# Kernel optimization log

Measured on AMD Instinct MI355X. Metric: run time of the kernel, lower is better.

The kernel has to match this reference:

```python
import jax, jax.numpy as jnp
import numpy as np

T, B, E, H = 2048, 2, 2048, 16
HD = E // H
SCALE = HD ** -0.5
NEG = -1e9  # large-negative additive mask (finite, safe in fp32/bf16)


def setup_inputs() -> dict:
    key = jax.random.key(0)
    ks = jax.random.split(key, 6)
    query = jax.random.normal(ks[0], (T, B, E), dtype=jnp.float32)
    # causal additive mask, as metaseq builds for decoder self-attention
    attn_mask = jnp.where(jnp.tril(jnp.ones((T, T), dtype=bool)), 0.0, NEG).astype(jnp.float32)
    # combined qkv projection: rows ordered [K | V | Q] per split_tensor_along_last_dim
    qkv_w = jax.random.normal(ks[1], (3 * E, E), dtype=jnp.float32) * (1.0 / np.sqrt(2 * E))
    qkv_b = jax.random.uniform(ks[2], (3 * E,), dtype=jnp.float32, minval=-1, maxval=1) / np.sqrt(E)
    out_w = jax.random.normal(ks[3], (E, E), dtype=jnp.float32) * (1.0 / np.sqrt(2 * E))
    out_b = jax.random.uniform(ks[4], (E,), dtype=jnp.float32, minval=-1, maxval=1) / np.sqrt(E)
    return {"query": query, "attn_mask": attn_mask, "qkv_w": qkv_w,
            "qkv_b": qkv_b, "out_w": out_w, "out_b": out_b}


def reference(query, attn_mask, qkv_w, qkv_b, out_w, out_b):
    t, b, e = query.shape
    # fused QKV projection (ColumnParallelLinear, world_size=1)
    kvq = jnp.einsum('tbe,fe->tbf', query, qkv_w) + qkv_b  # [T,B,3E]
    k, v, q = kvq[..., :e], kvq[..., e:2 * e], kvq[..., 2 * e:]
    q = q * SCALE
    q = q.reshape(t, b, H, HD)
    k = k.reshape(t, b, H, HD)
    v = v.reshape(t, b, H, HD)
    # explicit QK^T bmm -> [B,H,T,S]
    scores = jnp.einsum('tbhd,sbhd->bhts', q, k) + attn_mask[None, None]
    probs = jax.nn.softmax(scores, axis=-1)  # dropout p=0 -> identity
    ctx = jnp.einsum('bhts,sbhd->tbhd', probs, v).reshape(t, b, e)
    # RowParallelLinear out_proj (skip_bias_add in the original; bias added here)
    out = jnp.einsum('tbe,fe->tbf', ctx, out_w) + out_b
    return out
```

## Files before the change

### kernel.cpp

```cpp
#include <hip/hip_runtime.h>
#include <hip/hip_bf16.h>
#include <stdint.h>

#define T_DIM 2048
#define B_DIM 2
#define E_DIM 2048
#define H_DIM 16
#define HD_DIM 128
#define F_DIM 6144
#define F2   4096
#define ROWS 4096
#define KVB 64

#define QK_SCALE 0.08838834764831845f
#define LOG2E    1.4426950408889634f
#define RESCALE_THR 8.0f

typedef __bf16 bf16_t;
typedef __bf16 bf16x8 __attribute__((ext_vector_type(8)));
typedef __bf16 bf16x4 __attribute__((ext_vector_type(4)));
typedef float  f32x4  __attribute__((ext_vector_type(4)));

__device__ __forceinline__ void gll16(const void* g, void* l) {
  __builtin_amdgcn_global_load_lds((const __attribute__((address_space(1))) void*)g,
                                   (__attribute__((address_space(3))) void*)l, 16, 0, 0);
}

__global__ void cvt3(const float* __restrict__ s0, bf16_t* __restrict__ d0, int n0,
                     const float* __restrict__ s1, bf16_t* __restrict__ d1, int n1,
                     const float* __restrict__ s2, bf16_t* __restrict__ d2, int n2) {
  int total = n0 + n1 + n2;
  int i = blockIdx.x * blockDim.x + threadIdx.x;
  int stride = gridDim.x * blockDim.x;
  for (; i < total; i += stride) {
    const float* s; bf16_t* d; int j;
    if (i < n0)            { s = s0; d = d0; j = i; }
    else if (i < n0 + n1)  { s = s1; d = d1; j = i - n0; }
    else                   { s = s2; d = d2; j = i - n0 - n1; }
    float4 v = ((const float4*)s)[j];
    bf16x4 o;
    o[0] = (bf16_t)v.x; o[1] = (bf16_t)v.y; o[2] = (bf16_t)v.z; o[3] = (bf16_t)v.w;
    ((bf16x4*)d)[j] = o;
  }
}

__launch_bounds__(256, 2)
__global__ void gemm_qkv(const bf16_t* __restrict__ A, const bf16_t* __restrict__ Bm,
                         const float* __restrict__ bias, bf16_t* __restrict__ KVQ2,
                         bf16_t* __restrict__ VTg)
{
  __shared__ __align__(16) bf16_t Sm[2][128][64];
  bf16_t* Tp = &Sm[0][0][0];
  const int K = E_DIM, nbn = 48;

  int bid = blockIdx.x;
  int cpx = gridDim.x >> 3;
  int swz = (bid & 7) * cpx + (bid >> 3);
  int bm = swz / nbn, bn = swz % nbn;

  int tid = threadIdx.x;
  int lane = tid & 63, wid = tid >> 6;
  int lr = lane & 15, lg = lane >> 4;
  int wm = wid >> 1, wn = wid & 1;

  f32x4 acc[4][4] = {};

  int srow8 = tid >> 3;
  int schunk = tid & 7;

  const bf16_t* gA = A + (size_t)(bm * 128) * K;
  const bf16_t* gB = Bm + (size_t)(bn * 128) * K;

  for (int k0 = 0; k0 < K; k0 += 64) {
    #pragma unroll
    for (int i = 0; i < 4; ++i) {
      int row = i * 32 + srow8;
      int sc = schunk ^ (row & 7);
      gll16(gA + (size_t)row * K + k0 + sc * 8, &Sm[0][row][schunk * 8]);
    }
    #pragma unroll
    for (int i = 0; i < 4; ++i) {
      int row = i * 32 + srow8;
      int sc = schunk ^ (row & 7);
      gll16(gB + (size_t)row * K + k0 + sc * 8, &Sm[1][row][schunk * 8]);
    }
    __syncthreads();

    #pragma unroll
    for (int kk = 0; kk < 2; ++kk) {
      bf16x8 af[4], bfr[4];
      #pragma unroll
      for (int mi = 0; mi < 4; ++mi) {
        int row = wm * 64 + mi * 16 + lr;
        int ch = (kk * 4 + lg) ^ (row & 7);
        af[mi] = *(const bf16x8*)&Sm[0][row][ch * 8];
      }
      #pragma unroll
      for (int ni = 0; ni < 4; ++ni) {
        int row = wn * 64 + ni * 16 + lr;
        int ch = (kk * 4 + lg) ^ (row & 7);
        bfr[ni] = *(const bf16x8*)&Sm[1][row][ch * 8];
      }
      #pragma unroll
      for (int mi = 0; mi < 4; ++mi)
        #pragma unroll
        for (int ni = 0; ni < 4; ++ni)
          acc[mi][ni] = __builtin_amdgcn_mfma_f32_16x16x32_bf16(af[mi], bfr[ni], acc[mi][ni], 0, 0, 0);
    }
    __syncthreads();
  }

  if (bn >= 16 && bn < 32) {
    int h = bn - 16;
    #pragma unroll
    for (int mi = 0; mi < 4; ++mi) {
      int row0 = wm * 64 + mi * 16 + lg * 4;
      #pragma unroll
      for (int ni = 0; ni < 4; ++ni) {
        int lc = wn * 64 + ni * 16 + lr;
        float bv = bias[bn * 128 + lc];
        bf16x4 pk;
        #pragma unroll
        for (int r = 0; r < 4; ++r) pk[r] = (bf16_t)(acc[mi][ni][r] + bv);
        int rowX = row0 ^ ((lc & 15) << 3);
        *(bf16x4*)&Tp[lc * 128 + rowX] = pk;
      }
    }
    __syncthreads();
    int d = tid >> 1, half = tid & 1;
    int sz = (d & 15) << 3;
    size_t tb = (size_t)bm * 64 + half * 32;
    bf16_t* o0 = VTg + ((size_t)h        * 128 + d) * T_DIM + tb;
    bf16_t* o1 = VTg + ((size_t)(16 + h) * 128 + d) * T_DIM + tb;
    #pragma unroll
    for (int kk = 0; kk < 4; ++kk) {
      int rl = half * 64 + kk * 16;
      bf16x8 v0 = *(const bf16x8*)&Tp[d * 128 + ((rl)     ^ sz)];
      bf16x8 v1 = *(const bf16x8*)&Tp[d * 128 + ((rl + 8) ^ sz)];
      bf16x8 ev, od;
      #pragma unroll
      for (int j = 0; j < 4; ++j) {
        ev[j] = v0[2 * j];     ev[4 + j] = v1[2 * j];
        od[j] = v0[2 * j + 1]; od[4 + j] = v1[2 * j + 1];
      }
      *(bf16x8*)(o0 + kk * 8) = ev;
      *(bf16x8*)(o1 + kk * 8) = od;
    }
  } else {
    bool isQ = (bn >= 32);
    float scl = isQ ? (QK_SCALE * LOG2E) : 1.0f;
    int colOff = isQ ? -2048 : 0;
    #pragma unroll
    for (int mi = 0; mi < 4; ++mi) {
      int row0 = bm * 128 + wm * 64 + mi * 16 + lg * 4;
      #pragma unroll
      for (int ni = 0; ni < 4; ++ni) {
        int col = bn * 128 + wn * 64 + ni * 16 + lr;
        float bv = bias[col];
        #pragma unroll
        for (int r = 0; r < 4; ++r) {
          float v = (acc[mi][ni][r] + bv) * scl;
          KVQ2[(size_t)(row0 + r) * F2 + col + colOff] = (bf16_t)v;
        }
      }
    }
  }
}

__launch_bounds__(256, 2)
__global__ void gemm_out(const bf16_t* __restrict__ A, const bf16_t* __restrict__ Bm,
                         const float* __restrict__ bias, float* __restrict__ Cout)
{
  __shared__ __align__(16) bf16_t As[128][64];
  __shared__ __align__(16) bf16_t Bs[128][64];
  const int K = E_DIM, N = E_DIM, nbn = 16;

  int bid = blockIdx.x;
  int cpx = gridDim.x >> 3;
  int swz = (bid & 7) * cpx + (bid >> 3);
  int bm = swz / nbn, bn = swz % nbn;

  int tid = threadIdx.x;
  int lane = tid & 63, wid = tid >> 6;
  int lr = lane & 15, lg = lane >> 4;
  int wm = wid >> 1, wn = wid & 1;

  f32x4 acc[4][4] = {};
  int srow8 = tid >> 3, schunk = tid & 7;

  const bf16_t* gA = A + (size_t)(bm * 128) * K;
  const bf16_t* gB = Bm + (size_t)(bn * 128) * K;

  for (int k0 = 0; k0 < K; k0 += 64) {
    #pragma unroll
    for (int i = 0; i < 4; ++i) {
      int row = i * 32 + srow8;
      int sc = schunk ^ (row & 7);
      gll16(gA + (size_t)row * K + k0 + sc * 8, &As[row][schunk * 8]);
    }
    #pragma unroll
    for (int i = 0; i < 4; ++i) {
      int row = i * 32 + srow8;
      int sc = schunk ^ (row & 7);
      gll16(gB + (size_t)row * K + k0 + sc * 8, &Bs[row][schunk * 8]);
    }
    __syncthreads();

    #pragma unroll
    for (int kk = 0; kk < 2; ++kk) {
      bf16x8 af[4], bfr[4];
      #pragma unroll
      for (int mi = 0; mi < 4; ++mi) {
        int row = wm * 64 + mi * 16 + lr;
        int ch = (kk * 4 + lg) ^ (row & 7);
        af[mi] = *(const bf16x8*)&As[row][ch * 8];
      }
      #pragma unroll
      for (int ni = 0; ni < 4; ++ni) {
        int row = wn * 64 + ni * 16 + lr;
        int ch = (kk * 4 + lg) ^ (row & 7);
        bfr[ni] = *(const bf16x8*)&Bs[row][ch * 8];
      }
      #pragma unroll
      for (int mi = 0; mi < 4; ++mi)
        #pragma unroll
        for (int ni = 0; ni < 4; ++ni)
          acc[mi][ni] = __builtin_amdgcn_mfma_f32_16x16x32_bf16(af[mi], bfr[ni], acc[mi][ni], 0, 0, 0);
    }
    __syncthreads();
  }

  #pragma unroll
  for (int mi = 0; mi < 4; ++mi) {
    int row0 = bm * 128 + wm * 64 + mi * 16 + lg * 4;
    #pragma unroll
    for (int ni = 0; ni < 4; ++ni) {
      int col = bn * 128 + wn * 64 + ni * 16 + lr;
      float bv = bias[col];
      #pragma unroll
      for (int r = 0; r < 4; ++r)
        Cout[(size_t)(row0 + r) * N + col] = acc[mi][ni][r] + bv;
    }
  }
}

__launch_bounds__(256, 2)
__global__ void attn3(const bf16_t* __restrict__ KVQ2, const bf16_t* __restrict__ VTg,
                      bf16_t* __restrict__ CTX)
{
  __shared__ __align__(16) bf16_t Ks[2][KVB][128];
  __shared__ __align__(16) bf16_t Vs[2][128][KVB];
  __shared__ __align__(16) bf16_t Ps[4][32 * 64];

  int bid = blockIdx.x;
  int xcd = bid & 7;
  int j   = bid >> 3;
  int hi  = j >> 5;
  int mid = (j >> 4) & 1;
  int q   = j & 15;
  int bh  = xcd * 4 + hi * 2 + mid;
  int qt  = hi ? (15 - q) : q;
  int b = bh >> 4, h = bh & 15;

  int tid = threadIdx.x;
  int lane = tid & 63, wid = tid >> 6;
  int lr = lane & 15, lg = lane >> 4;

  const bf16_t* kbase = KVQ2 + (size_t)b * F2 + (size_t)h * HD_DIM;
  const bf16_t* vtb   = VTg + (size_t)bh * HD_DIM * T_DIM;
  bf16_t* PsW = &Ps[wid][0];

  bf16x8 qf[2][4];
  #pragma unroll
  for (int mf = 0; mf < 2; ++mf) {
    int t = qt * 128 + wid * 32 + mf * 16 + lr;
    const bf16_t* qb = KVQ2 + ((size_t)t * B_DIM + b) * F2 + E_DIM + h * HD_DIM;
    #pragma unroll
    for (int ks = 0; ks < 4; ++ks) qf[mf][ks] = *(const bf16x8*)(qb + ks * 32 + lg * 8);
  }

  f32x4 ctxa[2][8] = {};
  float m[2][4], lsum[2][4];
  #pragma unroll
  for (int mf = 0; mf < 2; ++mf)
    #pragma unroll
    for (int r = 0; r < 4; ++r) { m[mf][r] = -1e30f; lsum[mf][r] = 0.0f; }

  int krow = tid >> 4, kch = tid & 15;
  int vrow = tid >> 3, vch = tid & 7;

  auto stage = [&](int buf, int it) {
    int s0 = it * KVB;
    #pragma unroll
    for (int i = 0; i < 4; ++i) {
      int row = i * 16 + krow;
      int sc = kch ^ (row & 7);
      gll16(kbase + (size_t)(s0 + row) * B_DIM * F2 + sc * 8, &Ks[buf][row][kch * 8]);
    }
    #pragma unroll
    for (int i = 0; i < 4; ++i) {
      int row = i * 32 + vrow;
      int sc = vch ^ (row & 7);
      gll16(vtb + (size_t)row * T_DIM + s0 + sc * 8, &Vs[buf][row][vch * 8]);
    }
  };

  int nt = 2 * (qt + 1);
  stage(0, 0);
  __syncthreads();

  int tqw = qt * 128 + wid * 32;

  for (int it = 0; it < nt; ++it) {
    int cur = it & 1;
    if (it + 1 < nt) stage(cur ^ 1, it + 1);
    int s0 = it * KVB;
    bool diag = (it >= nt - 2);

    f32x4 sacc[2][4] = {};
    __builtin_amdgcn_s_setprio(1);
    #pragma unroll
    for (int ks = 0; ks < 4; ++ks) {
      #pragma unroll
      for (int nti = 0; nti < 4; ++nti) {
        int srow = nti * 16 + lr;
        int slot = (ks * 4 + lg) ^ (srow & 7);
        bf16x8 kf = *(const bf16x8*)&Ks[cur][srow][slot * 8];
        sacc[0][nti] = __builtin_amdgcn_mfma_f32_16x16x32_bf16(qf[0][ks], kf, sacc[0][nti], 0, 0, 0);
        sacc[1][nti] = __builtin_amdgcn_mfma_f32_16x16x32_bf16(qf[1][ks], kf, sacc[1][nti], 0, 0, 0);
      }
    }
    __builtin_amdgcn_s_setprio(0);

    float mxl = -1e30f;
    #pragma unroll
    for (int mf = 0; mf < 2; ++mf)
      #pragma unroll
      for (int r = 0; r < 4; ++r)
        #pragma unroll
        for (int nti = 0; nti < 4; ++nti) {
          float v = sacc[mf][nti][r];
          if (diag) v = (s0 + nti * 16 + lr > tqw + mf * 16 + lg * 4 + r) ? -1e30f : v;
          sacc[mf][nti][r] = v;
          mxl = fmaxf(mxl, v - m[mf][r]);
        }
    if (!__all(mxl <= RESCALE_THR)) {
      #pragma unroll
      for (int mf = 0; mf < 2; ++mf)
        #pragma unroll
        for (int r = 0; r < 4; ++r) {
          float mx = fmaxf(fmaxf(sacc[mf][0][r], sacc[mf][1][r]),
                           fmaxf(sacc[mf][2][r], sacc[mf][3][r]));
          #pragma unroll
          for (int d = 1; d < 16; d <<= 1) mx = fmaxf(mx, __shfl_xor(mx, d, 64));
          float mn = fmaxf(m[mf][r], mx);
          float rs = exp2f(m[mf][r] - mn);
          m[mf][r] = mn;
          lsum[mf][r] *= rs;
          #pragma unroll
          for (int dt = 0; dt < 8; ++dt) ctxa[mf][dt][r] *= rs;
        }
    }
    #pragma unroll
    for (int mf = 0; mf < 2; ++mf)
      #pragma unroll
      for (int r = 0; r < 4; ++r) {
        int prow = mf * 16 + lg * 4 + r;
        #pragma unroll
        for (int nti = 0; nti < 4; ++nti) {
          float p = exp2f(sacc[mf][nti][r] - m[mf][r]);
          lsum[mf][r] += p;
          int chk = (nti * 2 + (lr >> 3)) ^ (prow & 7);
          PsW[prow * 64 + chk * 8 + (lr & 7)] = (bf16_t)p;
        }
      }
    asm volatile("s_waitcnt lgkmcnt(0)" ::: "memory");
    __builtin_amdgcn_sched_barrier(0);

    bf16x8 pf[2][2];
    #pragma unroll
    for (int mf = 0; mf < 2; ++mf) {
      int prow = mf * 16 + lr;
      #pragma unroll
      for (int kh = 0; kh < 2; ++kh) {
        int chk = (kh * 4 + lg) ^ (prow & 7);
        pf[mf][kh] = *(const bf16x8*)&PsW[prow * 64 + chk * 8];
      }
    }
    __builtin_amdgcn_s_setprio(1);
    #pragma unroll
    for (int dt = 0; dt < 8; ++dt) {
      int drow = dt * 16 + lr;
      int sl0 = lg ^ (drow & 7);
      int sl1 = (4 + lg) ^ (drow & 7);
      bf16x8 vf0 = *(const bf16x8*)&Vs[cur][drow][sl0 * 8];
      bf16x8 vf1 = *(const bf16x8*)&Vs[cur][drow][sl1 * 8];
      ctxa[0][dt] = __builtin_amdgcn_mfma_f32_16x16x32_bf16(pf[0][0], vf0, ctxa[0][dt], 0, 0, 0);
      ctxa[0][dt] = __builtin_amdgcn_mfma_f32_16x16x32_bf16(pf[0][1], vf1, ctxa[0][dt], 0, 0, 0);
      ctxa[1][dt] = __builtin_amdgcn_mfma_f32_16x16x32_bf16(pf[1][0], vf0, ctxa[1][dt], 0, 0, 0);
      ctxa[1][dt] = __builtin_amdgcn_mfma_f32_16x16x32_bf16(pf[1][1], vf1, ctxa[1][dt], 0, 0, 0);
    }
    __builtin_amdgcn_s_setprio(0);

    __syncthreads();
  }

  #pragma unroll
  for (int mf = 0; mf < 2; ++mf)
    #pragma unroll
    for (int r = 0; r < 4; ++r) {
      #pragma unroll
      for (int d = 1; d < 16; d <<= 1) lsum[mf][r] += __shfl_xor(lsum[mf][r], d, 64);
    }

  #pragma unroll
  for (int mf = 0; mf < 2; ++mf)
    #pragma unroll
    for (int r = 0; r < 4; ++r) {
      int t = qt * 128 + wid * 32 + mf * 16 + lg * 4 + r;
      float inv = 1.0f / lsum[mf][r];
      bf16_t* out = CTX + ((size_t)t * B_DIM + b) * E_DIM + h * HD_DIM;
      #pragma unroll
      for (int dt = 0; dt < 8; ++dt)
        out[dt * 16 + lr] = (bf16_t)(ctxa[mf][dt][r] * inv);
    }
}

extern "C" void kernel_launch(void* const* d_in, const int* in_sizes, int n_in,
                              void* d_out, int out_size, void* d_ws, size_t ws_size,
                              hipStream_t stream)
{
  const float* query = (const float*)d_in[0];
  const float* qkv_w = (const float*)d_in[2];
  const float* qkv_b = (const float*)d_in[3];
  const float* out_w = (const float*)d_in[4];
  const float* out_b = (const float*)d_in[5];

  bf16_t* Xbf  = (bf16_t*)d_ws;
  bf16_t* Wqkv = Xbf  + (size_t)ROWS * E_DIM;
  bf16_t* Wout = Wqkv + (size_t)F_DIM * E_DIM;
  bf16_t* KVQ2 = Wout + (size_t)E_DIM * E_DIM;
  bf16_t* VTg  = KVQ2 + (size_t)ROWS * F2;
  bf16_t* CTX  = Xbf;

  cvt3<<<2048, 256, 0, stream>>>(query, Xbf,  ROWS * E_DIM / 4,
                                 qkv_w, Wqkv, F_DIM * E_DIM / 4,
                                 out_w, Wout, E_DIM * E_DIM / 4);

  gemm_qkv<<<32 * 48, 256, 0, stream>>>(Xbf, Wqkv, qkv_b, KVQ2, VTg);

  attn3<<<512, 256, 0, stream>>>(KVQ2, VTg, CTX);

  gemm_out<<<32 * 16, 256, 0, stream>>>(CTX, Wout, out_b, (float*)d_out);
}
```

Before: 269.9 us.

## Swap MFMA operand order so each lane owns one query row in attention

```diff
diff --git a/kernel.cpp b/kernel.cpp
--- a/kernel.cpp
+++ b/kernel.cpp
@@ -245,12 +245,12 @@
 }
 
 __launch_bounds__(256, 2)
-__global__ void attn3(const bf16_t* __restrict__ KVQ2, const bf16_t* __restrict__ VTg,
+__global__ void attn4(const bf16_t* __restrict__ KVQ2, const bf16_t* __restrict__ VTg,
                       bf16_t* __restrict__ CTX)
 {
   __shared__ __align__(16) bf16_t Ks[2][KVB][128];
   __shared__ __align__(16) bf16_t Vs[2][128][KVB];
-  __shared__ __align__(16) bf16_t Ps[4][32 * 64];
+  __shared__ __align__(16) bf16_t Ps[4][2][16][64];
 
   int bid = blockIdx.x;
   int xcd = bid & 7;
@@ -268,7 +268,6 @@
 
   const bf16_t* kbase = KVQ2 + (size_t)b * F2 + (size_t)h * HD_DIM;
   const bf16_t* vtb   = VTg + (size_t)bh * HD_DIM * T_DIM;
-  bf16_t* PsW = &Ps[wid][0];
 
   bf16x8 qf[2][4];
   #pragma unroll
@@ -280,11 +279,8 @@
   }
 
   f32x4 ctxa[2][8] = {};
-  float m[2][4], lsum[2][4];
-  #pragma unroll
-  for (int mf = 0; mf < 2; ++mf)
-    #pragma unroll
-    for (int r = 0; r < 4; ++r) { m[mf][r] = -1e30f; lsum[mf][r] = 0.0f; }
+  float mR[2] = { -1e30f, -1e30f };
+  float lR[2] = { 0.0f, 0.0f };
 
   int krow = tid >> 4, kch = tid & 15;
   int vrow = tid >> 3, vch = tid & 7;
@@ -326,67 +322,69 @@
         int srow = nti * 16 + lr;
         int slot = (ks * 4 + lg) ^ (srow & 7);
         bf16x8 kf = *(const bf16x8*)&Ks[cur][srow][slot * 8];
-        sacc[0][nti] = __builtin_amdgcn_mfma_f32_16x16x32_bf16(qf[0][ks], kf, sacc[0][nti], 0, 0, 0);
-        sacc[1][nti] = __builtin_amdgcn_mfma_f32_16x16x32_bf16(qf[1][ks], kf, sacc[1][nti], 0, 0, 0);
+        sacc[0][nti] = __builtin_amdgcn_mfma_f32_16x16x32_bf16(kf, qf[0][ks], sacc[0][nti], 0, 0, 0);
+        sacc[1][nti] = __builtin_amdgcn_mfma_f32_16x16x32_bf16(kf, qf[1][ks], sacc[1][nti], 0, 0, 0);
       }
     }
     __builtin_amdgcn_s_setprio(0);
 
     float mxl = -1e30f;
     #pragma unroll
+    for (int mf = 0; mf < 2; ++mf) {
+      int qg = tqw + mf * 16 + lr;
+      #pragma unroll
+      for (int nti = 0; nti < 4; ++nti)
+        #pragma unroll
+        for (int r = 0; r < 4; ++r) {
+          float v = sacc[mf][nti][r];
+          if (diag) v = (s0 + nti * 16 + lg * 4 + r > qg) ? -1e30f : v;
+          sacc[mf][nti][r] = v;
+          mxl = fmaxf(mxl, v - mR[mf]);
+        }
+    }
+    if (!__all(mxl <= RESCALE_THR)) {
+      #pragma unroll
+      for (int mf = 0; mf < 2; ++mf) {
+        float mx = -1e30f;
+        #pragma unroll
+        for (int nti = 0; nti < 4; ++nti)
+          #pragma unroll
+          for (int r = 0; r < 4; ++r) mx = fmaxf(mx, sacc[mf][nti][r]);
+        mx = fmaxf(mx, __shfl_xor(mx, 16, 64));
+        mx = fmaxf(mx, __shfl_xor(mx, 32, 64));
+        float mn = fmaxf(mR[mf], mx);
+        float rs = exp2f(mR[mf] - mn);
+        mR[mf] = mn;
+        lR[mf] *= rs;
+        #pragma unroll
+        for (int dt = 0; dt < 8; ++dt) ctxa[mf][dt] *= rs;
+      }
+    }
+    #pragma unroll
     for (int mf = 0; mf < 2; ++mf)
       #pragma unroll
-      for (int r = 0; r < 4; ++r)
-        #pragma unroll
-        for (int nti = 0; nti < 4; ++nti) {
-          float v = sacc[mf][nti][r];
-          if (diag) v = (s0 + nti * 16 + lr > tqw + mf * 16 + lg * 4 + r) ? -1e30f : v;
-          sacc[mf][nti][r] = v;
-          mxl = fmaxf(mxl, v - m[mf][r]);
+      for (int nti = 0; nti < 4; ++nti) {
+        bf16x4 pk;
+        float ps = 0.0f;
+        #pragma unroll
+        for (int r = 0; r < 4; ++r) {
+          float p = exp2f(sacc[mf][nti][r] - mR[mf]);
+          ps += p;
+          pk[r] = (bf16_t)p;
         }
-    if (!__all(mxl <= RESCALE_THR)) {
-      #pragma unroll
-      for (int mf = 0; mf < 2; ++mf)
-        #pragma unroll
-        for (int r = 0; r < 4; ++r) {
-          float mx = fmaxf(fmaxf(sacc[mf][0][r], sacc[mf][1][r]),
-                           fmaxf(sacc[mf][2][r], sacc[mf][3][r]));
-          #pragma unroll
-          for (int d = 1; d < 16; d <<= 1) mx = fmaxf(mx, __shfl_xor(mx, d, 64));
-          float mn = fmaxf(m[mf][r], mx);
-          float rs = exp2f(m[mf][r] - mn);
-          m[mf][r] = mn;
-          lsum[mf][r] *= rs;
-          #pragma unroll
-          for (int dt = 0; dt < 8; ++dt) ctxa[mf][dt][r] *= rs;
-        }
-    }
-    #pragma unroll
-    for (int mf = 0; mf < 2; ++mf)
-      #pragma unroll
-      for (int r = 0; r < 4; ++r) {
-        int prow = mf * 16 + lg * 4 + r;
-        #pragma unroll
-        for (int nti = 0; nti < 4; ++nti) {
-          float p = exp2f(sacc[mf][nti][r] - m[mf][r]);
-          lsum[mf][r] += p;
-          int chk = (nti * 2 + (lr >> 3)) ^ (prow & 7);
-          PsW[prow * 64 + chk * 8 + (lr & 7)] = (bf16_t)p;
-        }
+        lR[mf] += ps;
+        int cS = (nti * 2 + (lg >> 1)) ^ (lr & 7);
+        *(bf16x4*)&Ps[wid][mf][lr][cS * 8 + (lg & 1) * 4] = pk;
       }
     asm volatile("s_waitcnt lgkmcnt(0)" ::: "memory");
     __builtin_amdgcn_sched_barrier(0);
 
-    bf16x8 pf[2][2];
-    #pragma unroll
-    for (int mf = 0; mf < 2; ++mf) {
-      int prow = mf * 16 + lr;
-      #pragma unroll
-      for (int kh = 0; kh < 2; ++kh) {
-        int chk = (kh * 4 + lg) ^ (prow & 7);
-        pf[mf][kh] = *(const bf16x8*)&PsW[prow * 64 + chk * 8];
-      }
-    }
+    bf16x8 pb[2][2];
+    #pragma unroll
+    for (int mf = 0; mf < 2; ++mf)
+      #pragma unroll
+      for (int kh = 0; kh < 2; ++kh)
+        pb[mf][kh] = *(const bf16x8*)&Ps[wid][mf][lr][(((kh * 4 + lg)) ^ (lr & 7)) * 8];
     __builtin_amdgcn_s_setprio(1);
     #pragma unroll
     for (int dt = 0; dt < 8; ++dt) {
@@ -395,10 +393,10 @@
       int sl1 = (4 + lg) ^ (drow & 7);
       bf16x8 vf0 = *(const bf16x8*)&Vs[cur][drow][sl0 * 8];
       bf16x8 vf1 = *(const bf16x8*)&Vs[cur][drow][sl1 * 8];
-      ctxa[0][dt] = __builtin_amdgcn_mfma_f32_16x16x32_bf16(pf[0][0], vf0, ctxa[0][dt], 0, 0, 0);
-      ctxa[0][dt] = __builtin_amdgcn_mfma_f32_16x16x32_bf16(pf[0][1], vf1, ctxa[0][dt], 0, 0, 0);
-      ctxa[1][dt] = __builtin_amdgcn_mfma_f32_16x16x32_bf16(pf[1][0], vf0, ctxa[1][dt], 0, 0, 0);
-      ctxa[1][dt] = __builtin_amdgcn_mfma_f32_16x16x32_bf16(pf[1][1], vf1, ctxa[1][dt], 0, 0, 0);
+      ctxa[0][dt] = __builtin_amdgcn_mfma_f32_16x16x32_bf16(vf0, pb[0][0], ctxa[0][dt], 0, 0, 0);
+      ctxa[0][dt] = __builtin_amdgcn_mfma_f32_16x16x32_bf16(vf1, pb[0][1], ctxa[0][dt], 0, 0, 0);
+      ctxa[1][dt] = __builtin_amdgcn_mfma_f32_16x16x32_bf16(vf0, pb[1][0], ctxa[1][dt], 0, 0, 0);
+      ctxa[1][dt] = __builtin_amdgcn_mfma_f32_16x16x32_bf16(vf1, pb[1][1], ctxa[1][dt], 0, 0, 0);
     }
     __builtin_amdgcn_s_setprio(0);
 
@@ -406,24 +404,20 @@
   }
 
   #pragma unroll
-  for (int mf = 0; mf < 2; ++mf)
-    #pragma unroll
-    for (int r = 0; r < 4; ++r) {
-      #pragma unroll
-      for (int d = 1; d < 16; d <<= 1) lsum[mf][r] += __shfl_xor(lsum[mf][r], d, 64);
-    }
-
-  #pragma unroll
-  for (int mf = 0; mf < 2; ++mf)
-    #pragma unroll
-    for (int r = 0; r < 4; ++r) {
-      int t = qt * 128 + wid * 32 + mf * 16 + lg * 4 + r;
-      float inv = 1.0f / lsum[mf][r];
-      bf16_t* out = CTX + ((size_t)t * B_DIM + b) * E_DIM + h * HD_DIM;
-      #pragma unroll
-      for (int dt = 0; dt < 8; ++dt)
-        out[dt * 16 + lr] = (bf16_t)(ctxa[mf][dt][r] * inv);
-    }
+  for (int mf = 0; mf < 2; ++mf) {
+    lR[mf] += __shfl_xor(lR[mf], 16, 64);
+    lR[mf] += __shfl_xor(lR[mf], 32, 64);
+    float inv = 1.0f / lR[mf];
+    int t = tqw + mf * 16 + lr;
+    bf16_t* out = CTX + ((size_t)t * B_DIM + b) * E_DIM + h * HD_DIM;
+    #pragma unroll
+    for (int dt = 0; dt < 8; ++dt) {
+      bf16x4 pk;
+      #pragma unroll
+      for (int r = 0; r < 4; ++r) pk[r] = (bf16_t)(ctxa[mf][dt][r] * inv);
+      *(bf16x4*)(out + dt * 16 + lg * 4) = pk;
+    }
+  }
 }
 
 extern "C" void kernel_launch(void* const* d_in, const int* in_sizes, int n_in,
@@ -449,7 +443,7 @@
 
   gemm_qkv<<<32 * 48, 256, 0, stream>>>(Xbf, Wqkv, qkv_b, KVQ2, VTg);
 
-  attn3<<<512, 256, 0, stream>>>(KVQ2, VTg, CTX);
+  attn4<<<512, 256, 0, stream>>>(KVQ2, VTg, CTX);
 
   gemm_out<<<32 * 16, 256, 0, stream>>>(CTX, Wout, out_b, (float*)d_out);
 }
```

Measured after the change: 265.7 us, median of 3. About the same (-1.6%).
